# Kernel tuning notes

Measured on AMD Instinct MI355X. Metric: run time of the kernel, lower is better.

The kernel has to match this reference:

```python
import jax, jax.numpy as jnp
import numpy as np

T, B, D, R, S, M, H = 1024, 4, 1024, 64, 16, 64, 16
NEG_INF = -1e8


def setup_inputs() -> dict:
    key = jax.random.key(0)
    ks = jax.random.split(key, 12)
    Q, K = R + T + S, M + R + T
    inp = {
        "utterance": jax.random.normal(ks[0], (T, B, D), jnp.float32),
        "right_context": jax.random.normal(ks[1], (R, B, D), jnp.float32),
        "summary": jax.random.normal(ks[2], (S, B, D), jnp.float32),
        "mems": jax.random.normal(ks[3], (M, B, D), jnp.float32),
        # valid frame counts in [1, T]; ensure at least one element == T so
        # max(lengths) stresses the full utterance span
        "lengths": jnp.asarray(
            jax.random.randint(ks[4], (B,), 1, T + 1).at[0].set(T), jnp.int32
        ),
        "attention_mask": jax.random.uniform(ks[5], (Q, K)) < 0.1,
        # Linear params stored as (in, out); y = x @ W + b  (== torch Linear)
        "Wq": jax.random.normal(ks[6], (D, D), jnp.float32) * 0.02,
        "bq": jnp.zeros((D,), jnp.float32),
        "Wkv": jax.random.normal(ks[7], (D, 2 * D), jnp.float32) * 0.02,
        "bkv": jnp.zeros((2 * D,), jnp.float32),
        "Wout": jax.random.normal(ks[8], (D, D), jnp.float32) * 0.02,
        "bout": jnp.zeros((D,), jnp.float32),
    }
    return inp


def reference(utterance, right_context, summary, mems, lengths, attention_mask,
              Wq, bq, Wkv, bkv, Wout, bout):
    d_head = D // H
    scaling = d_head ** -0.5
    Q = R + T + S  # query length
    Kl = M + R + T  # key length (non-streaming)

    # projections
    query = jnp.concatenate([right_context, utterance, summary], axis=0) @ Wq + bq  # (Q,B,D)
    kv = jnp.concatenate([mems, right_context, utterance], axis=0) @ Wkv + bkv      # (K,B,2D)
    k, v = jnp.split(kv, 2, axis=2)  # each (K,B,D)

    # (L, B, D) -> (B*H, L, d_head), matching torch view+transpose
    def heads(x):
        return x.reshape(x.shape[0], B * H, d_head).swapaxes(0, 1)

    qh, kh, vh = heads(query), heads(k), heads(v)

    # fp32 scores + masking, as in the original (masked_fill in float)
    w = jnp.einsum("nqd,nkd->nqk", qh * scaling, kh).astype(jnp.float32)  # (B*H,Q,K)
    w = jnp.where(attention_mask[None, :, :], NEG_INF, w)

    # padding mask over keys: klengths = lengths + M + (R+T - max(lengths))
    klengths = lengths + M + R + T - jnp.max(lengths)
    pad = jnp.arange(Kl, dtype=lengths.dtype)[None, :] >= klengths[:, None]  # (B,K)
    w = w.reshape(B, H, Q, Kl)
    w = jnp.where(pad[:, None, None, :], NEG_INF, w)
    w = w.reshape(B * H, Q, Kl)

    probs = jax.nn.softmax(w, axis=-1).astype(utterance.dtype)  # dropout p=0.0

    attn = jnp.einsum("nqk,nkd->nqd", probs, vh)          # (B*H,Q,d)
    attn = attn.swapaxes(0, 1).reshape(Q, B, D)           # (Q,B,D)
    out = attn @ Wout + bout

    output = out[: Q - S]                 # right_context + utterance outputs
    output_mems = jnp.tanh(out[Q - S:])   # summary -> new mems
    out_key = k[M + R:]                   # utterance keys for streaming cache
    out_val = v[M + R:]
    return output, output_mems, out_key, out_val
```

## Files before the change

kernel.cpp:

```cpp
#include <hip/hip_runtime.h>
#include <hip/hip_bf16.h>

typedef __attribute__((ext_vector_type(8))) short short8;
typedef __attribute__((ext_vector_type(4))) float f32x4;

#define DEV __device__ __forceinline__

constexpr int Tn = 1024, Bn = 4, Dn = 1024, Rn = 64, Sn = 16, Mn = 64, Hn = 16;
constexpr int DH = 64;
constexpr int Qn = Rn + Tn + Sn;
constexpr int KL = Mn + Rn + Tn;
constexpr int NT = KL / 64;
constexpr int NQB = 18;
constexpr int QB = Qn * Bn;
constexpr int KB = KL * Bn;
constexpr int MU = 4672;
constexpr size_t OUTM = (size_t)(Rn + Tn) * Bn * Dn;
constexpr size_t OUTK = OUTM + (size_t)Sn * Bn * Dn;
constexpr size_t OUTV = OUTK + (size_t)Tn * Bn * Dn;
constexpr size_t NU  = (size_t)Tn * Bn * Dn;
constexpr size_t NR_ = (size_t)Rn * Bn * Dn;
constexpr size_t NS_ = (size_t)Sn * Bn * Dn;
constexpr size_t NM_ = (size_t)Mn * Bn * Dn;
constexpr float QSCALE = 0.18033688f;

DEV float b2f(ushort u) { union { unsigned v; float f; } x; x.v = ((unsigned)u) << 16; return x.f; }
DEV ushort f2b(float f) { __hip_bfloat16 h = __float2bfloat16(f); return *reinterpret_cast<ushort*>(&h); }

DEV float ldbias(const void* p, int i, int fp32) {
    return fp32 ? ((const float*)p)[i] : b2f(((const ushort*)p)[i]);
}
DEV void stout(void* p, size_t i, float v, int fp32) {
    if (fp32) ((float*)p)[i] = v; else ((ushort*)p)[i] = f2b(v);
}
DEV bool mread(const void* m, size_t idx, int mode) {
    if (mode == 0) return ((const unsigned char*)m)[idx] != 0;
    if (mode == 1) return ((const int*)m)[idx] != 0;
    return ((const float*)m)[idx] != 0.f;
}

DEV void gload_lds16(const void* g, void* l) {
    __builtin_amdgcn_global_load_lds(
        (const __attribute__((address_space(1))) unsigned int*)g,
        (__attribute__((address_space(3))) unsigned int*)l, 16, 0, 0);
}

DEV unsigned cvt_pk_bf16(float lo, float hi) {
    unsigned r;
    asm("v_cvt_pk_bf16_f32 %0, %1, %2" : "=v"(r) : "v"(lo), "v"(hi));
    return r;
}

DEV int sigma_key(int v) {
    return (2 * (v >> 5) + ((v & 7) >> 2)) * 16 + ((v >> 3) & 3) * 4 + (v & 3);
}

__global__ __launch_bounds__(256) void probe_kernel(const ushort* utt, const unsigned char* mask,
                                                    int* flags) {
    __shared__ int cnt[4];
    if (threadIdx.x < 4) cnt[threadIdx.x] = 0;
    __syncthreads();
    int c = 0;
    for (int i = threadIdx.x; i < 2048; i += 256) {
        int e = (utt[i] >> 7) & 0xFF;
        if (e > 64 && e < 192) c++;
    }
    atomicAdd(&cnt[0], c);
    int c0 = 0, c1 = 0, c23 = 0;
    for (int i = threadIdx.x; i < 8192; i += 256) {
        if (mask[i]) { int m = i & 3; if (m == 0) c0++; else if (m == 1) c1++; else c23++; }
    }
    atomicAdd(&cnt[1], c0); atomicAdd(&cnt[2], c1); atomicAdd(&cnt[3], c23);
    __syncthreads();
    if (threadIdx.x == 0) {
        flags[0] = (cnt[0] < 1900) ? 1 : 0;
        int mmode;
        if (cnt[2] == 0 && cnt[3] == 0) mmode = 1;
        else if (cnt[1] == 0) mmode = 2;
        else mmode = 0;
        flags[1] = mmode;
    }
}

__global__ __launch_bounds__(256) void build_mbits(const void* __restrict__ amask,
                                                   const int* __restrict__ lengths,
                                                   unsigned long long* __restrict__ mbits,
                                                   const int* __restrict__ flags) {
    const int mmode = flags[1];
    int word = blockIdx.x * 4 + (threadIdx.x >> 6);
    if (word >= Bn * Qn * NT) return;
    int lane = threadIdx.x & 63;
    int ktl = word % NT;
    int rem = word / NT;
    int q = rem % Qn;
    int b = rem / Qn;
    const int l0 = lengths[0], l1 = lengths[1], l2 = lengths[2], l3 = lengths[3];
    const int maxlen = max(max(l0, l1), max(l2, l3));
    const int klen = lengths[b] + KL - maxlen;
    int kg = ktl * 64 + lane;
    bool m = mread(amask, (size_t)q * KL + kg, mmode) || (kg >= klen);
    unsigned long long bal = __ballot(m);
    if (lane == 0) mbits[word] = bal;
}

__global__ __launch_bounds__(256) void convert_acts(const void* utt, const void* rc,
                                                    const void* sm, const void* mm,
                                                    ushort* dst, const int* flags) {
    const int fp32 = flags[0];
    const size_t total = (NU + NR_ + NS_ + NM_) / 8;
    for (size_t cidx = (size_t)blockIdx.x * 256 + threadIdx.x; cidx < total;
         cidx += (size_t)gridDim.x * 256) {
        size_t e = cidx * 8; const void* src; size_t li; ushort* d;
        if (e < NU)                  { src = utt; li = e;                 d = dst; }
        else if (e < NU + NR_)       { src = rc;  li = e - NU;            d = dst + NU; }
        else if (e < NU + NR_ + NS_) { src = sm;  li = e - NU - NR_;      d = dst + NU + NR_; }
        else                         { src = mm;  li = e - NU - NR_ - NS_; d = dst + NU + NR_ + NS_; }
        if (fp32) {
            const float* f = (const float*)src + li;
            ushort o[8];
#pragma unroll
            for (int j = 0; j < 8; ++j) o[j] = f2b(f[j]);
            *(short8*)(d + li) = *(short8*)o;
        } else {
            *(short8*)(d + li) = *(const short8*)((const ushort*)src + li);
        }
    }
}

__global__ __launch_bounds__(256) void transpose_w3(const void* Wq, const void* Wkv, const void* Wout,
                                                    ushort* WqT, ushort* WkvT, ushort* WoutT,
                                                    const int* flags) {
    __shared__ alignas(16) ushort tile[64 * 64];
    const int fp32 = flags[0];
    const int z = blockIdx.z;
    const void* W; ushort* WT; int N;
    int tc = blockIdx.x, tr = blockIdx.y;
    if (z == 0)      { W = Wq;   WT = WqT;   N = 1024; }
    else if (z == 3) { W = Wout; WT = WoutT; N = 1024; }
    else             { W = Wkv;  WT = WkvT;  N = 2048; tc += (z - 1) * 16; }
    const int K = 1024;
    const int t = threadIdx.x;
    for (int c = t; c < 512; c += 256) {
        int row = c >> 3, q = c & 7;
        int u = q ^ (row & 7);
        ushort o[8];
#pragma unroll
        for (int j = 0; j < 8; ++j) {
            size_t gi = (size_t)(tr * 64 + row) * N + tc * 64 + q * 8 + j;
            o[j] = fp32 ? f2b(((const float*)W)[gi]) : ((const ushort*)W)[gi];
        }
        *(short8*)&tile[row * 64 + u * 8] = *(short8*)o;
    }
    __syncthreads();
    for (int c = t; c < 512; c += 256) {
        int n = c >> 3, q = c & 7;
        ushort vv[8];
#pragma unroll
        for (int j = 0; j < 8; ++j) {
            int k = q * 8 + j;
            int u = (n >> 3) ^ (k & 7);
            vv[j] = tile[k * 64 + u * 8 + (n & 7)];
        }
        *(short8*)(WT + (size_t)(tc * 64 + n) * K + tr * 64 + q * 8) = *(short8*)vv;
    }
}

__global__ __launch_bounds__(256) void transpose_v(const ushort* __restrict__ kv,
                                                   ushort* __restrict__ vT) {
    __shared__ alignas(16) ushort tile[64 * 64];
    const int kt = blockIdx.x, bh = blockIdx.y;
    const int b = bh >> 4, h = bh & 15;
    const int t = threadIdx.x;
    for (int c = t; c < 512; c += 256) {
        int key = c >> 3, q = c & 7;
        short8 v = *(const short8*)(kv + ((size_t)(kt * 64 + key) * Bn + b) * 2048 + 1024 + h * DH + q * 8);
        int u = q ^ (key & 7);
        *(short8*)&tile[key * 64 + u * 8] = v;
    }
    __syncthreads();
    for (int c = t; c < 512; c += 256) {
        int d = c >> 3, q = c & 7;
        ushort vv[8];
#pragma unroll
        for (int j = 0; j < 8; ++j) {
            int key = sigma_key(q * 8 + j);
            int u = (d >> 3) ^ (key & 7);
            vv[j] = tile[key * 64 + u * 8 + (d & 7)];
        }
        *(short8*)(vT + ((size_t)bh * 64 + d) * KL + kt * 64 + q * 8) = *(short8*)vv;
    }
}

#define Q128_STAGE(DSTBUF, KT)                                                        \
    _Pragma("unroll")                                                                 \
    for (int i2 = 0; i2 < 4; ++i2) {                                                  \
        gload_lds16(asrc[i2] + (KT) * 64, &As[DSTBUF][(i2 * 256 + t) * 8]);           \
        gload_lds16(bsrc[i2] + (KT) * 64, &Bs[DSTBUF][(i2 * 256 + t) * 8]);           \
    }

__global__ __launch_bounds__(256, 2) void gemm_qkv(
    const ushort* __restrict__ cmem, const ushort* __restrict__ crc,
    const ushort* __restrict__ cutt, const ushort* __restrict__ csum,
    const ushort* __restrict__ Bt, const void* __restrict__ bq, const void* __restrict__ bkv,
    ushort* __restrict__ q_ws, ushort* __restrict__ kv_ws,
    void* __restrict__ gout, const int* __restrict__ flags) {
    __shared__ alignas(16) ushort As[2][8192];
    __shared__ alignas(16) ushort Bs[2][8192];
    const int ofp = flags[0];
    const int t = threadIdx.x;
    const int lane = t & 63;
    const int w = t >> 6;
    const int wr = w >> 1, wc = w & 1;
    const int g = lane >> 4, lr = lane & 15;

    const int bid = blockIdx.x;
    const int wg = (bid & 7) * 111 + (bid >> 3);
    const int bx = wg % 24, by = wg / 24;
    const int mbase = by * 128, nbase = bx * 128;

    const ushort* asrc[4]; const ushort* bsrc[4];
#pragma unroll
    for (int i2 = 0; i2 < 4; ++i2) {
        int slot = i2 * 256 + t;
        int row = slot >> 3, kc = slot & 7;
        int q = kc ^ (row & 7);
        int grow = mbase + row;
        if (grow >= MU) grow = MU - 1;
        const ushort* s;
        if (grow < 256)       s = cmem + (size_t)grow * 1024;
        else if (grow < 512)  s = crc + (size_t)(grow - 256) * 1024;
        else if (grow < 4608) s = cutt + (size_t)(grow - 512) * 1024;
        else                  s = csum + (size_t)(grow - 4608) * 1024;
        asrc[i2] = s + q * 8;
        bsrc[i2] = Bt + (size_t)(nbase + row) * 1024 + q * 8;
    }

    f32x4 acc[4][4] = {};

    Q128_STAGE(0, 0);

    for (int kt = 0; kt < 16; ++kt) {
        const int c = kt & 1;
        if (kt + 1 < 16) {
            Q128_STAGE(c ^ 1, kt + 1);
            asm volatile("s_waitcnt vmcnt(8)" ::: "memory");
        } else {
            asm volatile("s_waitcnt vmcnt(0)" ::: "memory");
        }
        __builtin_amdgcn_sched_barrier(0);
        __builtin_amdgcn_s_barrier();

        short8 bfr[4][2];
#pragma unroll
        for (int n = 0; n < 4; ++n)
#pragma unroll
            for (int ks = 0; ks < 2; ++ks) {
                int col = wc * 64 + n * 16 + lr;
                bfr[n][ks] = *(const short8*)&Bs[c][col * 64 + (((ks * 4 + g) ^ (lr & 7)) << 3)];
            }
        short8 af[4][2];
#pragma unroll
        for (int m = 0; m < 4; ++m)
#pragma unroll
            for (int ks = 0; ks < 2; ++ks) {
                int row = wr * 64 + m * 16 + lr;
                af[m][ks] = *(const short8*)&As[c][row * 64 + (((ks * 4 + g) ^ (lr & 7)) << 3)];
            }
        __builtin_amdgcn_s_setprio(1);
#pragma unroll
        for (int m = 0; m < 4; ++m)
#pragma unroll
            for (int n = 0; n < 4; ++n) {
                acc[m][n] = __builtin_amdgcn_mfma_f32_16x16x32_bf16(af[m][0], bfr[n][0], acc[m][n], 0, 0, 0);
                acc[m][n] = __builtin_amdgcn_mfma_f32_16x16x32_bf16(af[m][1], bfr[n][1], acc[m][n], 0, 0, 0);
            }
        __builtin_amdgcn_s_setprio(0);

        __builtin_amdgcn_sched_barrier(0);
        __builtin_amdgcn_s_barrier();
    }

#pragma unroll
    for (int n = 0; n < 4; ++n) {
        int col = nbase + wc * 64 + n * 16 + lr;
        float bv = (col < 1024) ? ldbias(bq, col, ofp) : ldbias(bkv, col - 1024, ofp);
#pragma unroll
        for (int m = 0; m < 4; ++m) {
            int rowb = mbase + wr * 64 + m * 16 + g * 4;
#pragma unroll
            for (int i = 0; i < 4; ++i) {
                int r = rowb + i;
                if (r >= MU) continue;
                float val = acc[m][n][i] + bv;
                if (col < 1024) {
                    if (r >= 256) q_ws[(size_t)(r - 256) * 1024 + col] = f2b(val * QSCALE);
                } else {
                    if (r < 4608) {
                        kv_ws[(size_t)r * 2048 + (col - 1024)] = f2b(val);
                        if (r >= 512) {
                            size_t o = (col < 2048)
                                ? OUTK + (size_t)(r - 512) * 1024 + (col - 1024)
                                : OUTV + (size_t)(r - 512) * 1024 + (col - 2048);
                            stout(gout, o, val, ofp);
                        }
                    }
                }
            }
        }
    }
}

#define O_STAGE(DSTBUF, KT)                                                           \
    _Pragma("unroll")                                                                 \
    for (int i2 = 0; i2 < 2; ++i2)                                                    \
        gload_lds16(asrc[i2] + (KT) * 64, &As[DSTBUF][(i2 * 256 + t) * 8]);           \
    _Pragma("unroll")                                                                 \
    for (int i2 = 0; i2 < 4; ++i2)                                                    \
        gload_lds16(bsrc[i2] + (KT) * 64, &Bs[DSTBUF][(i2 * 256 + t) * 8]);

__global__ __launch_bounds__(256, 3) void gemm_out(
    const ushort* __restrict__ A, const ushort* __restrict__ Bt,
    const void* __restrict__ bias, void* __restrict__ gout, const int* __restrict__ flags) {
    __shared__ alignas(16) ushort As[2][4096];
    __shared__ alignas(16) ushort Bs[2][8192];
    const int ofp = flags[0];
    const int t = threadIdx.x;
    const int lane = t & 63;
    const int w = t >> 6;
    const int wr = w >> 1, wc = w & 1;
    const int g = lane >> 4, lr = lane & 15;

    const int nwg = gridDim.x;
    const int bid = blockIdx.x;
    const int wg = (bid & 7) * (nwg >> 3) + (bid >> 3);
    const int bx = wg % 8, by = wg / 8;
    const int mbase = by * 64, nbase = bx * 128;

    const ushort* asrc[2];
#pragma unroll
    for (int i2 = 0; i2 < 2; ++i2) {
        int slot = i2 * 256 + t;
        int row = slot >> 3, kc = slot & 7, q = kc ^ (row & 7);
        asrc[i2] = A + (size_t)(mbase + row) * 1024 + q * 8;
    }
    const ushort* bsrc[4];
#pragma unroll
    for (int i2 = 0; i2 < 4; ++i2) {
        int slot = i2 * 256 + t;
        int row = slot >> 3, kc = slot & 7, q = kc ^ (row & 7);
        bsrc[i2] = Bt + (size_t)(nbase + row) * 1024 + q * 8;
    }

    f32x4 acc[2][4] = {};

    O_STAGE(0, 0);

    for (int kt = 0; kt < 16; ++kt) {
        const int c = kt & 1;
        if (kt + 1 < 16) {
            O_STAGE(c ^ 1, kt + 1);
            asm volatile("s_waitcnt vmcnt(6)" ::: "memory");
        } else {
            asm volatile("s_waitcnt vmcnt(0)" ::: "memory");
        }
        __builtin_amdgcn_sched_barrier(0);
        __builtin_amdgcn_s_barrier();

        short8 bfr[4][2];
#pragma unroll
        for (int n = 0; n < 4; ++n)
#pragma unroll
            for (int ks = 0; ks < 2; ++ks) {
                int col = wc * 64 + n * 16 + lr;
                bfr[n][ks] = *(const short8*)&Bs[c][col * 64 + (((ks * 4 + g) ^ (lr & 7)) << 3)];
            }
        short8 af[2][2];
#pragma unroll
        for (int m = 0; m < 2; ++m)
#pragma unroll
            for (int ks = 0; ks < 2; ++ks) {
                int row = wr * 32 + m * 16 + lr;
                af[m][ks] = *(const short8*)&As[c][row * 64 + (((ks * 4 + g) ^ (lr & 7)) << 3)];
            }
        __builtin_amdgcn_s_setprio(1);
#pragma unroll
        for (int m = 0; m < 2; ++m)
#pragma unroll
            for (int n = 0; n < 4; ++n) {
                acc[m][n] = __builtin_amdgcn_mfma_f32_16x16x32_bf16(af[m][0], bfr[n][0], acc[m][n], 0, 0, 0);
                acc[m][n] = __builtin_amdgcn_mfma_f32_16x16x32_bf16(af[m][1], bfr[n][1], acc[m][n], 0, 0, 0);
            }
        __builtin_amdgcn_s_setprio(0);

        __builtin_amdgcn_sched_barrier(0);
        __builtin_amdgcn_s_barrier();
    }

#pragma unroll
    for (int n = 0; n < 4; ++n) {
        int col = nbase + wc * 64 + n * 16 + lr;
        float bv = ldbias(bias, col, ofp);
#pragma unroll
        for (int m = 0; m < 2; ++m) {
            int rowb = mbase + wr * 32 + m * 16 + g * 4;
#pragma unroll
            for (int i = 0; i < 4; ++i) {
                int row = rowb + i;
                float val = acc[m][n][i] + bv;
                if (row < (Rn + Tn) * Bn) stout(gout, (size_t)row * 1024 + col, val, ofp);
                else stout(gout, OUTM + (size_t)(row - (Rn + Tn) * Bn) * 1024 + col, tanhf(val), ofp);
            }
        }
    }
}

#define ATTN_STAGE(DSTBUF, KT)                                                        \
    gload_lds16(ksrc0 + (size_t)(KT) * kstep, &Ks[DSTBUF][w * 1024]);                 \
    gload_lds16(ksrc1 + (size_t)(KT) * kstep, &Ks[DSTBUF][w * 1024 + 512]);           \
    gload_lds16(vsrc0 + (size_t)(KT) * 64,    &Vs[DSTBUF][w * 1024]);                 \
    gload_lds16(vsrc1 + (size_t)(KT) * 64,    &Vs[DSTBUF][w * 1024 + 512]);

#define ATTN_PHASE(CUR, WBCUR, PRE, KTN, WBNXT, VMSTR)                                \
    {                                                                                 \
        if (PRE) { ATTN_STAGE((CUR) ^ 1, KTN); WBNXT = mp[KTN]; }                     \
        asm volatile("s_waitcnt " VMSTR ::: "memory");                                \
        __builtin_amdgcn_sched_barrier(0);                                            \
        __builtin_amdgcn_s_barrier();                                                 \
        __builtin_amdgcn_sched_barrier(0);                                            \
        f32x4 sa[4] = {};                                                             \
        __builtin_amdgcn_s_setprio(1);                                                \
        _Pragma("unroll")                                                             \
        for (int n = 0; n < 4; ++n) {                                                 \
            int key = n * 16 + lr;                                                    \
            short8 kb0 = *(const short8*)&Ks[CUR][key * 64 + ((g ^ (key & 7)) << 3)]; \
            short8 kb1 = *(const short8*)&Ks[CUR][key * 64 + (((4 + g) ^ (key & 7)) << 3)]; \
            sa[n] = __builtin_amdgcn_mfma_f32_16x16x32_bf16(kb0, qf0, sa[n], 0, 0, 0); \
            sa[n] = __builtin_amdgcn_mfma_f32_16x16x32_bf16(kb1, qf1, sa[n], 0, 0, 0); \
        }                                                                             \
        __builtin_amdgcn_s_setprio(0);                                                \
        unsigned pkk[4][2];                                                           \
        _Pragma("unroll")                                                             \
        for (int n = 0; n < 4; ++n) {                                                 \
            unsigned bits = (unsigned)((WBCUR) >> (n * 16 + g * 4)) & 15u;            \
            float p[4];                                                               \
            _Pragma("unroll")                                                         \
            for (int i = 0; i < 4; ++i) {                                             \
                float sv = ((bits >> i) & 1u) ? -100.0f : sa[n][i];                   \
                p[i] = exp2f(sv);                                                     \
                lsum += p[i];                                                         \
            }                                                                         \
            pkk[n][0] = cvt_pk_bf16(p[0], p[1]);                                      \
            pkk[n][1] = cvt_pk_bf16(p[2], p[3]);                                      \
        }                                                                             \
        union { unsigned u[4]; short8 s; } c0, c1;                                    \
        c0.u[0] = pkk[0][0]; c0.u[1] = pkk[0][1]; c0.u[2] = pkk[1][0]; c0.u[3] = pkk[1][1]; \
        c1.u[0] = pkk[2][0]; c1.u[1] = pkk[2][1]; c1.u[2] = pkk[3][0]; c1.u[3] = pkk[3][1]; \
        __builtin_amdgcn_s_setprio(1);                                                \
        _Pragma("unroll")                                                             \
        for (int n = 0; n < 4; ++n) {                                                 \
            int d = n * 16 + lr;                                                      \
            short8 vb0 = *(const short8*)&Vs[CUR][d * 64 + ((g ^ (d & 7)) << 3)];     \
            short8 vb1 = *(const short8*)&Vs[CUR][d * 64 + (((4 + g) ^ (d & 7)) << 3)]; \
            acc_o[n] = __builtin_amdgcn_mfma_f32_16x16x32_bf16(c0.s, vb0, acc_o[n], 0, 0, 0); \
            acc_o[n] = __builtin_amdgcn_mfma_f32_16x16x32_bf16(c1.s, vb1, acc_o[n], 0, 0, 0); \
        }                                                                             \
        __builtin_amdgcn_s_setprio(0);                                                \
        __builtin_amdgcn_sched_barrier(0);                                            \
        __builtin_amdgcn_s_barrier();                                                 \
    }

__global__ __launch_bounds__(256, 5) void attn_kernel(
    const ushort* __restrict__ qws, const ushort* __restrict__ kvws, const ushort* __restrict__ vTws,
    const unsigned long long* __restrict__ mbits,
    ushort* __restrict__ attnws) {
    __shared__ alignas(16) ushort Ks[2][64 * 64];
    __shared__ alignas(16) ushort Vs[2][64 * 64];

    const int bid = blockIdx.x;
    const int wg = (bid & 7) * (gridDim.x >> 3) + (bid >> 3);
    const int qblk = wg % NQB;
    const int bh = wg / NQB;
    const int b = bh >> 4, h = bh & 15;
    const int t = threadIdx.x;
    const int w = t >> 6, lane = t & 63;
    const int g = lane >> 4, lr = lane & 15;

    const int qi = qblk * 64 + w * 16 + lr;
    const int qic = qi < Qn ? qi : (Qn - 1);
    const ushort* qptr = qws + ((size_t)qic * Bn + b) * Dn + h * DH;
    const short8 qf0 = *(const short8*)(qptr + g * 8);
    const short8 qf1 = *(const short8*)(qptr + 32 + g * 8);
    const unsigned long long* mp = mbits + ((size_t)b * Qn + qic) * NT;

    const int srow0 = w * 16 + (lane >> 3);
    const int srow1 = srow0 + 8;
    const int sw = (((lane & 7) ^ ((lane >> 3) & 7)) << 3);
    const ushort* ksrc0 = kvws + ((size_t)srow0 * Bn + b) * 2048 + h * DH + sw;
    const ushort* ksrc1 = kvws + ((size_t)srow1 * Bn + b) * 2048 + h * DH + sw;
    const ushort* vsrc0 = vTws + ((size_t)bh * 64 + srow0) * KL + sw;
    const ushort* vsrc1 = vTws + ((size_t)bh * 64 + srow1) * KL + sw;
    const size_t kstep = (size_t)64 * Bn * 2048;

    f32x4 acc_o[4] = {};
    float lsum = 0.f;
    unsigned long long wbA, wbB;

    ATTN_STAGE(0, 0);
    wbA = mp[0];
    wbB = 0;

    for (int kt2 = 0; kt2 < NT - 2; kt2 += 2) {
        ATTN_PHASE(0, wbA, true, kt2 + 1, wbB, "vmcnt(5)");
        ATTN_PHASE(1, wbB, true, kt2 + 2, wbA, "vmcnt(5)");
    }
    ATTN_PHASE(0, wbA, true, NT - 1, wbB, "vmcnt(5)");
    ATTN_PHASE(1, wbB, false, 0, wbA, "vmcnt(0)");

    float ls = lsum;
    ls += __shfl_xor(ls, 16);
    ls += __shfl_xor(ls, 32);
#pragma unroll
    for (int i = 0; i < 4; ++i) {
        int qrow = g * 4 + i;
        float lsv = __shfl(ls, (lane & 48) | qrow);
        int qg = qblk * 64 + w * 16 + qrow;
        if (qg >= Qn) continue;
        float inv = 1.f / lsv;
#pragma unroll
        for (int n = 0; n < 4; ++n) {
            attnws[((size_t)qg * Bn + b) * Dn + h * DH + n * 16 + lr] = f2b(acc_o[n][i] * inv);
        }
    }
}

extern "C" void kernel_launch(void* const* d_in, const int* in_sizes, int n_in,
                              void* d_out, int out_size, void* d_ws, size_t ws_size,
                              hipStream_t stream) {
    const void* utt   = d_in[0];
    const void* rc    = d_in[1];
    const void* summ  = d_in[2];
    const void* mems  = d_in[3];
    const int*  lens  = (const int*)d_in[4];
    const void* amask = d_in[5];
    const void* Wq   = d_in[6];
    const void* bq   = d_in[7];
    const void* Wkv  = d_in[8];
    const void* bkv  = d_in[9];
    const void* Wout = d_in[10];
    const void* bout = d_in[11];

    ushort* ws    = (ushort*)d_ws;
    int*   flags  = (int*)d_ws;
    ushort* cu    = ws + 64;
    ushort* cutt  = cu;
    ushort* crc   = cutt + NU;
    ushort* csum  = crc + NR_;
    ushort* cmem  = csum + NS_;
    ushort* WqT   = cmem + NM_;
    ushort* WkvT  = WqT + (size_t)1024 * 1024;
    ushort* WoutT = WkvT + (size_t)2048 * 1024;
    ushort* q_ws  = WoutT + (size_t)1024 * 1024;
    ushort* kv_ws = q_ws + (size_t)QB * Dn;
    ushort* vT_ws = kv_ws + (size_t)KB * 2048;
    ushort* at_ws = vT_ws + (size_t)64 * 64 * KL;
    unsigned long long* mbits = (unsigned long long*)(at_ws + (size_t)QB * Dn);

    probe_kernel<<<1, 256, 0, stream>>>((const ushort*)utt, (const unsigned char*)amask, flags);
    build_mbits<<<(Bn * Qn * NT + 3) / 4, 256, 0, stream>>>(amask, lens, mbits, flags);
    convert_acts<<<1024, 256, 0, stream>>>(utt, rc, summ, mems, cu, flags);
    transpose_w3<<<dim3(16, 16, 4), 256, 0, stream>>>(Wq, Wkv, Wout, WqT, WkvT, WoutT, flags);

    gemm_qkv<<<dim3(888), 256, 0, stream>>>(cmem, crc, cutt, csum, WqT, bq, bkv,
                                            q_ws, kv_ws, d_out, flags);
    transpose_v<<<dim3(KL / 64, Bn * Hn), 256, 0, stream>>>(kv_ws, vT_ws);
    attn_kernel<<<dim3(NQB * Bn * Hn), 256, 0, stream>>>(q_ws, kv_ws, vT_ws, mbits, at_ws);
    gemm_out<<<dim3(552), 256, 0, stream>>>(at_ws, WoutT, bout, d_out, flags);
}
```

Baseline: 182.9 us.

## Use 256x256 tiles with 8 waves and interleaved prefetch in QKV GEMM

The QKV projection GEMM moves from 128x128 tiles with 4 waves to 256x256 tiles with 8 waves per block, giving 228 blocks instead of 888, with an XCD-aware block remap. Each k-step is split into four phases, and each phase issues part of the next tile's global-to-LDS prefetch between its LDS fragment reads and its MFMAs. The aim is more operand reuse per byte loaded and better overlap of memory with compute. The cost is one block per CU, more barriers per k-step, and a larger LDS footprint (128KB double buffered), which may tail-balance poorly with 228 blocks on 256 CUs.

```diff
diff --git a/kernel.cpp b/kernel.cpp
--- a/kernel.cpp
+++ b/kernel.cpp
@@ -191,91 +191,117 @@
     }
 }
 
-#define Q128_STAGE(DSTBUF, KT)                                                        \
+#define Q8_STAGE_A(BUF, KT, HALF)                                                     \
     _Pragma("unroll")                                                                 \
-    for (int i2 = 0; i2 < 4; ++i2) {                                                  \
-        gload_lds16(asrc[i2] + (KT) * 64, &As[DSTBUF][(i2 * 256 + t) * 8]);           \
-        gload_lds16(bsrc[i2] + (KT) * 64, &Bs[DSTBUF][(i2 * 256 + t) * 8]);           \
-    }
-
-__global__ __launch_bounds__(256, 2) void gemm_qkv(
+    for (int i2 = 0; i2 < 2; ++i2)                                                    \
+        gload_lds16(asrc2[HALF][i2] + (KT) * 64, &As[BUF][(HALF) * 8192 + (i2 * 512 + t) * 8]);
+#define Q8_STAGE_B(BUF, KT, HALF)                                                     \
+    _Pragma("unroll")                                                                 \
+    for (int i2 = 0; i2 < 2; ++i2)                                                    \
+        gload_lds16(bsrc2[HALF][i2] + (KT) * 64, &Bs[BUF][(HALF) * 8192 + (i2 * 512 + t) * 8]);
+
+#define Q8_RD_AF(BUF, P)                                                              \
+    _Pragma("unroll")                                                                 \
+    for (int mq = 0; mq < 2; ++mq)                                                    \
+        _Pragma("unroll")                                                             \
+        for (int ks = 0; ks < 2; ++ks) {                                              \
+            int r_ = wr * 128 + (P) * 32 + mq * 16 + lr;                              \
+            af[mq][ks] = *(const short8*)&As[BUF][r_ * 64 + (((ks * 4 + g) ^ (r_ & 7)) << 3)]; \
+        }
+
+#define Q8_MM(P)                                                                      \
+    __builtin_amdgcn_s_barrier();                                                     \
+    asm volatile("s_waitcnt lgkmcnt(0)" ::: "memory");                                \
+    __builtin_amdgcn_sched_barrier(0);                                                \
+    __builtin_amdgcn_s_setprio(1);                                                    \
+    _Pragma("unroll")                                                                 \
+    for (int mq = 0; mq < 2; ++mq)                                                    \
+        _Pragma("unroll")                                                             \
+        for (int n = 0; n < 4; ++n) {                                                 \
+            acc[(P) * 2 + mq][n] = __builtin_amdgcn_mfma_f32_16x16x32_bf16(af[mq][0], bfr[n][0], acc[(P) * 2 + mq][n], 0, 0, 0); \
+            acc[(P) * 2 + mq][n] = __builtin_amdgcn_mfma_f32_16x16x32_bf16(af[mq][1], bfr[n][1], acc[(P) * 2 + mq][n], 0, 0, 0); \
+        }                                                                             \
+    __builtin_amdgcn_s_setprio(0);
+
+__global__ __launch_bounds__(512, 1) void gemm_qkv(
     const ushort* __restrict__ cmem, const ushort* __restrict__ crc,
     const ushort* __restrict__ cutt, const ushort* __restrict__ csum,
     const ushort* __restrict__ Bt, const void* __restrict__ bq, const void* __restrict__ bkv,
     ushort* __restrict__ q_ws, ushort* __restrict__ kv_ws,
     void* __restrict__ gout, const int* __restrict__ flags) {
-    __shared__ alignas(16) ushort As[2][8192];
-    __shared__ alignas(16) ushort Bs[2][8192];
+    __shared__ alignas(16) ushort As[2][16384];
+    __shared__ alignas(16) ushort Bs[2][16384];
     const int ofp = flags[0];
     const int t = threadIdx.x;
     const int lane = t & 63;
     const int w = t >> 6;
-    const int wr = w >> 1, wc = w & 1;
+    const int wr = w >> 2, wc = w & 3;
     const int g = lane >> 4, lr = lane & 15;
 
     const int bid = blockIdx.x;
-    const int wg = (bid & 7) * 111 + (bid >> 3);
-    const int bx = wg % 24, by = wg / 24;
-    const int mbase = by * 128, nbase = bx * 128;
-
-    const ushort* asrc[4]; const ushort* bsrc[4];
-#pragma unroll
-    for (int i2 = 0; i2 < 4; ++i2) {
-        int slot = i2 * 256 + t;
-        int row = slot >> 3, kc = slot & 7;
-        int q = kc ^ (row & 7);
-        int grow = mbase + row;
-        if (grow >= MU) grow = MU - 1;
-        const ushort* s;
-        if (grow < 256)       s = cmem + (size_t)grow * 1024;
-        else if (grow < 512)  s = crc + (size_t)(grow - 256) * 1024;
-        else if (grow < 4608) s = cutt + (size_t)(grow - 512) * 1024;
-        else                  s = csum + (size_t)(grow - 4608) * 1024;
-        asrc[i2] = s + q * 8;
-        bsrc[i2] = Bt + (size_t)(nbase + row) * 1024 + q * 8;
-    }
-
-    f32x4 acc[4][4] = {};
-
-    Q128_STAGE(0, 0);
+    const int xcd = bid & 7, idx = bid >> 3;
+    const int wg = (xcd < 4 ? xcd * 29 : 116 + (xcd - 4) * 28) + idx;
+    const int bx = wg % 12, by = wg / 12;
+    const int mbase = by * 256, nbase = bx * 256;
+
+    const ushort* asrc2[2][2]; const ushort* bsrc2[2][2];
+#pragma unroll
+    for (int half = 0; half < 2; ++half)
+#pragma unroll
+        for (int i2 = 0; i2 < 2; ++i2) {
+            int slot = i2 * 512 + t;
+            int row = slot >> 3, kc = slot & 7;
+            int q = kc ^ (row & 7);
+            int grow = mbase + half * 128 + row;
+            if (grow >= MU) grow = MU - 1;
+            const ushort* s;
+            if (grow < 256)       s = cmem + (size_t)grow * 1024;
+            else if (grow < 512)  s = crc + (size_t)(grow - 256) * 1024;
+            else if (grow < 4608) s = cutt + (size_t)(grow - 512) * 1024;
+            else                  s = csum + (size_t)(grow - 4608) * 1024;
+            asrc2[half][i2] = s + q * 8;
+            bsrc2[half][i2] = Bt + (size_t)(nbase + half * 128 + row) * 1024 + q * 8;
+        }
+
+    f32x4 acc[8][4] = {};
+    short8 bfr[4][2], af[2][2];
+
+    Q8_STAGE_A(0, 0, 0); Q8_STAGE_A(0, 0, 1);
+    Q8_STAGE_B(0, 0, 0); Q8_STAGE_B(0, 0, 1);
+    asm volatile("s_waitcnt vmcnt(0)" ::: "memory");
+    __builtin_amdgcn_sched_barrier(0);
+    __builtin_amdgcn_s_barrier();
 
     for (int kt = 0; kt < 16; ++kt) {
-        const int c = kt & 1;
-        if (kt + 1 < 16) {
-            Q128_STAGE(c ^ 1, kt + 1);
-            asm volatile("s_waitcnt vmcnt(8)" ::: "memory");
-        } else {
-            asm volatile("s_waitcnt vmcnt(0)" ::: "memory");
-        }
-        __builtin_amdgcn_sched_barrier(0);
+        const int c = kt & 1, o = c ^ 1;
+        const bool pre = (kt + 1 < 16);
+
+#pragma unroll
+        for (int n = 0; n < 4; ++n)
+#pragma unroll
+            for (int ks = 0; ks < 2; ++ks) {
+                int r_ = wc * 64 + n * 16 + lr;
+                bfr[n][ks] = *(const short8*)&Bs[c][r_ * 64 + (((ks * 4 + g) ^ (r_ & 7)) << 3)];
+            }
+        Q8_RD_AF(c, 0);
+        if (pre) { Q8_STAGE_A(o, kt + 1, 0); }
+        Q8_MM(0);
         __builtin_amdgcn_s_barrier();
 
-        short8 bfr[4][2];
-#pragma unroll
-        for (int n = 0; n < 4; ++n)
-#pragma unroll
-            for (int ks = 0; ks < 2; ++ks) {
-                int col = wc * 64 + n * 16 + lr;
-                bfr[n][ks] = *(const short8*)&Bs[c][col * 64 + (((ks * 4 + g) ^ (lr & 7)) << 3)];
-            }
-        short8 af[4][2];
-#pragma unroll
-        for (int m = 0; m < 4; ++m)
-#pragma unroll
-            for (int ks = 0; ks < 2; ++ks) {
-                int row = wr * 64 + m * 16 + lr;
-                af[m][ks] = *(const short8*)&As[c][row * 64 + (((ks * 4 + g) ^ (lr & 7)) << 3)];
-            }
-        __builtin_amdgcn_s_setprio(1);
-#pragma unroll
-        for (int m = 0; m < 4; ++m)
-#pragma unroll
-            for (int n = 0; n < 4; ++n) {
-                acc[m][n] = __builtin_amdgcn_mfma_f32_16x16x32_bf16(af[m][0], bfr[n][0], acc[m][n], 0, 0, 0);
-                acc[m][n] = __builtin_amdgcn_mfma_f32_16x16x32_bf16(af[m][1], bfr[n][1], acc[m][n], 0, 0, 0);
-            }
-        __builtin_amdgcn_s_setprio(0);
-
+        Q8_RD_AF(c, 1);
+        if (pre) { Q8_STAGE_A(o, kt + 1, 1); }
+        Q8_MM(1);
+        __builtin_amdgcn_s_barrier();
+
+        Q8_RD_AF(c, 2);
+        if (pre) { Q8_STAGE_B(o, kt + 1, 0); }
+        Q8_MM(2);
+        __builtin_amdgcn_s_barrier();
+
+        Q8_RD_AF(c, 3);
+        if (pre) { Q8_STAGE_B(o, kt + 1, 1); }
+        Q8_MM(3);
+        asm volatile("s_waitcnt vmcnt(0)" ::: "memory");
         __builtin_amdgcn_sched_barrier(0);
         __builtin_amdgcn_s_barrier();
     }
@@ -285,8 +311,8 @@
         int col = nbase + wc * 64 + n * 16 + lr;
         float bv = (col < 1024) ? ldbias(bq, col, ofp) : ldbias(bkv, col - 1024, ofp);
 #pragma unroll
-        for (int m = 0; m < 4; ++m) {
-            int rowb = mbase + wr * 64 + m * 16 + g * 4;
+        for (int m = 0; m < 8; ++m) {
+            int rowb = mbase + wr * 128 + m * 16 + g * 4;
 #pragma unroll
             for (int i = 0; i < 4; ++i) {
                 int r = rowb + i;
@@ -298,10 +324,10 @@
                     if (r < 4608) {
                         kv_ws[(size_t)r * 2048 + (col - 1024)] = f2b(val);
                         if (r >= 512) {
-                            size_t o = (col < 2048)
+                            size_t o2 = (col < 2048)
                                 ? OUTK + (size_t)(r - 512) * 1024 + (col - 1024)
                                 : OUTV + (size_t)(r - 512) * 1024 + (col - 2048);
-                            stout(gout, o, val, ofp);
+                            stout(gout, o2, val, ofp);
                         }
                     }
                 }
@@ -570,7 +596,7 @@
     convert_acts<<<1024, 256, 0, stream>>>(utt, rc, summ, mems, cu, flags);
     transpose_w3<<<dim3(16, 16, 4), 256, 0, stream>>>(Wq, Wkv, Wout, WqT, WkvT, WoutT, flags);
 
-    gemm_qkv<<<dim3(888), 256, 0, stream>>>(cmem, crc, cutt, csum, WqT, bq, bkv,
+    gemm_qkv<<<dim3(228), 512, 0, stream>>>(cmem, crc, cutt, csum, WqT, bq, bkv,
                                             q_ws, kv_ws, d_out, flags);
     transpose_v<<<dim3(KL / 64, Bn * Hn), 256, 0, stream>>>(kv_ws, vT_ws);
     attn_kernel<<<dim3(NQB * Bn * Hn), 256, 0, stream>>>(q_ws, kv_ws, vT_ws, mbits, at_ws);
```

New measurement: 199.8 us. 1.09x slower.
